# Kernel optimization log

Hardware: AMD Instinct MI355X
Metric: run time of the kernel (lower is better)

## Reference

```python
import jax, jax.numpy as jnp
import numpy as np

N_NODES = 200000
N_EDGES = 400000
N_GRAPHS = 4096
H = 300
L = 5
BN_EPS = 1e-5


def setup_inputs() -> dict:
    key = jax.random.key(0)
    ks = jax.random.split(key, 12)
    s = 0.05  # weight scale for numerical stability across 5 layers
    return {
        'x': jax.random.randint(ks[0], (N_NODES, 9), 0, 120),
        'edge_index': jax.random.randint(ks[1], (2, N_EDGES), 0, N_NODES),
        'edge_attr': jax.random.randint(ks[2], (N_EDGES, 3), 0, 16),
        'batch': jnp.sort(jax.random.randint(ks[3], (N_NODES,), 0, N_GRAPHS)),
        'atom_emb': jax.random.normal(ks[4], (9, 120, H), jnp.float32) * s,
        'bond_emb': jax.random.normal(ks[5], (L, 3, 16, H), jnp.float32) * s,
        'eps': jnp.zeros((L,), jnp.float32),
        'W1': jax.random.normal(ks[6], (L, H, 2 * H), jnp.float32) * s,
        'b1': jnp.zeros((L, 2 * H), jnp.float32),
        'bn_gamma': jnp.ones((L, 2 * H), jnp.float32),
        'bn_beta': jnp.zeros((L, 2 * H), jnp.float32),
        'bn_mean': jnp.zeros((L, 2 * H), jnp.float32),
        'bn_var': jnp.ones((L, 2 * H), jnp.float32),
        'W2': jax.random.normal(ks[7], (L, 2 * H, H), jnp.float32) * s,
        'b2': jnp.zeros((L, H), jnp.float32),
        'cls_W': jax.random.normal(ks[8], (H, 2), jnp.float32) * s,
        'cls_b': jnp.zeros((2,), jnp.float32),
    }


def reference(x, edge_index, edge_attr, batch, atom_emb, bond_emb, eps,
              W1, b1, bn_gamma, bn_beta, bn_mean, bn_var, W2, b2, cls_W, cls_b):
    N = x.shape[0]
    # AtomEncoder: sum of 9 categorical embeddings -> [N, H]
    h = jnp.sum(atom_emb[jnp.arange(9)[None, :], x], axis=1)
    src, dst = edge_index[0], edge_index[1]
    feat_idx3 = jnp.arange(3)[None, :]
    for l in range(W1.shape[0]):
        # BondEncoder for this layer: sum of 3 categorical embeddings -> [E, H]
        e = jnp.sum(bond_emb[l][feat_idx3, edge_attr], axis=1)
        # message = relu(x_j + edge_emb), aggregated by scatter-add at dst
        m = jax.nn.relu(h[src] + e)
        agg = jax.ops.segment_sum(m, dst, num_segments=N)
        z = (1.0 + eps[l]) * h + agg
        # MLP: Linear(H,2H) -> BN(eval) -> ReLU -> Linear(2H,H)
        z = z @ W1[l] + b1[l]
        z = (z - bn_mean[l]) * (bn_gamma[l] * jax.lax.rsqrt(bn_var[l] + BN_EPS)) + bn_beta[l]
        z = jax.nn.relu(z)
        h = z @ W2[l] + b2[l]
    # global mean pool over graphs
    sums = jax.ops.segment_sum(h, batch, num_segments=N_GRAPHS)
    counts = jax.ops.segment_sum(jnp.ones((N, 1), h.dtype), batch, num_segments=N_GRAPHS)
    graph_feature = sums / jnp.maximum(counts, 1.0)
    logits = graph_feature @ cls_W + cls_b
    return logits, graph_feature
```

## Files before the change

### kernel.cpp

```cpp
#include <hip/hip_runtime.h>
#include <hip/hip_bf16.h>

#define N_NODES 200000
#define N_EDGES 400000
#define N_GRAPHS 4096
#define HDIM 300
#define H2DIM 600
#define NLAYERS 5

typedef __hip_bfloat16 bf16;
typedef __attribute__((ext_vector_type(4))) short s16x4;
typedef __attribute__((ext_vector_type(8))) short s16x8;
typedef __attribute__((ext_vector_type(4))) float f32x4v;

__device__ inline short f2bf(float f) {
    __hip_bfloat16 b = __float2bfloat16(f);
    return *(short*)&b;
}
__device__ inline float bf2f(short s) {
    __hip_bfloat16 b = *(__hip_bfloat16*)&s;
    return __bfloat162float(b);
}

__global__ void diag_kernel(float* __restrict__ out, int n, float val) {
    int i = blockIdx.x * blockDim.x + threadIdx.x;
    if (i < n) out[i] = val;
}

__global__ void hist_kernel(const int* __restrict__ edge_index, int* __restrict__ offs) {
    int e = blockIdx.x * blockDim.x + threadIdx.x;
    if (e >= N_EDGES) return;
    atomicAdd(&offs[edge_index[N_EDGES + e]], 1);
}

#define SCAN_N 200001
__global__ void scan1_kernel(int* __restrict__ offs, int* __restrict__ bsum) {
    __shared__ int ls[256];
    int tid = threadIdx.x;
    int base = blockIdx.x * 1024 + tid * 4;
    int v[4];
#pragma unroll
    for (int j = 0; j < 4; j++) v[j] = (base + j < SCAN_N) ? offs[base + j] : 0;
    int t = v[0] + v[1] + v[2] + v[3];
    ls[tid] = t;
    __syncthreads();
    for (int off = 1; off < 256; off <<= 1) {
        int y = (tid >= off) ? ls[tid - off] : 0;
        __syncthreads();
        ls[tid] += y;
        __syncthreads();
    }
    int ex = ls[tid] - t;
#pragma unroll
    for (int j = 0; j < 4; j++) {
        if (base + j < SCAN_N) offs[base + j] = ex;
        ex += v[j];
    }
    if (tid == 255) bsum[blockIdx.x] = ls[255];
}

__global__ void scan2_kernel(int* __restrict__ bsum, int nb) {
    __shared__ int ls[256];
    int tid = threadIdx.x;
    int v = (tid < nb) ? bsum[tid] : 0;
    ls[tid] = v;
    __syncthreads();
    for (int off = 1; off < 256; off <<= 1) {
        int y = (tid >= off) ? ls[tid - off] : 0;
        __syncthreads();
        ls[tid] += y;
        __syncthreads();
    }
    if (tid < nb) bsum[tid] = ls[tid] - v;
}

__global__ void scan3_kernel(int* __restrict__ offs, const int* __restrict__ bsum) {
    int i = blockIdx.x * blockDim.x + threadIdx.x;
    if (i >= SCAN_N) return;
    offs[i] += bsum[i >> 10];
}

__global__ void scatter_kernel(const int* __restrict__ edge_index,
                               const int* __restrict__ edge_attr,
                               int* __restrict__ offs,
                               int* __restrict__ sidx) {
    int e = blockIdx.x * blockDim.x + threadIdx.x;
    if (e >= N_EDGES) return;
    int src = edge_index[e];
    int dst = edge_index[N_EDGES + e];
    int combo = edge_attr[e * 3 + 0] | (edge_attr[e * 3 + 1] << 4) | (edge_attr[e * 3 + 2] << 8);
    int pos = atomicAdd(&offs[dst], 1);
    sidx[pos] = src | (combo << 18);
}

__global__ void etab_kernel(const float* __restrict__ bond_l, short* __restrict__ etab) {
    int idx = blockIdx.x * blockDim.x + threadIdx.x;
    if (idx >= 4096 * 304) return;
    int combo = idx / 304;
    int c = idx - combo * 304;
    if (c >= HDIM) { etab[idx] = 0; return; }
    int a0 = combo & 15, a1 = (combo >> 4) & 15, a2 = combo >> 8;
    float v = bond_l[a0 * HDIM + c] + bond_l[16 * HDIM + a1 * HDIM + c]
            + bond_l[32 * HDIM + a2 * HDIM + c];
    etab[idx] = f2bf(v);
}

__global__ void prep_w_swz(const float* __restrict__ W1, const float* __restrict__ W2,
                           short* __restrict__ Wt1s, short* __restrict__ Wt2s) {
    int idx = blockIdx.x * blockDim.x + threadIdx.x;
    const int G1 = NLAYERS * 40 * 10 * 64;
    const int G2 = NLAYERS * 20 * 20 * 64;
    if (idx < G1) {
        int l = idx / (40 * 10 * 64);
        int r = idx - l * (40 * 10 * 64);
        int nt = r / (10 * 64);
        int r2 = r - nt * (10 * 64);
        int kb = r2 >> 6;
        int lane = r2 & 63;
        int n = nt * 16 + (lane & 15);
        int k0 = kb * 32 + (lane >> 4) * 8;
        s16x8 o;
#pragma unroll
        for (int j = 0; j < 8; j++) {
            int k = k0 + j;
            float v = (n < H2DIM && k < HDIM) ? W1[((size_t)l * HDIM + k) * H2DIM + n] : 0.f;
            o[j] = f2bf(v);
        }
        *(s16x8*)&Wt1s[(size_t)idx * 8] = o;
    } else if (idx < G1 + G2) {
        int t = idx - G1;
        int l = t / (20 * 20 * 64);
        int r = t - l * (20 * 20 * 64);
        int nt = r / (20 * 64);
        int r2 = r - nt * (20 * 64);
        int kb = r2 >> 6;
        int lane = r2 & 63;
        int n = nt * 16 + (lane & 15);
        int k0 = kb * 32 + (lane >> 4) * 8;
        s16x8 o;
#pragma unroll
        for (int j = 0; j < 8; j++) {
            int k = k0 + j;
            float v = (n < HDIM && k < H2DIM) ? W2[((size_t)l * H2DIM + k) * HDIM + n] : 0.f;
            o[j] = f2bf(v);
        }
        *(s16x8*)&Wt2s[(size_t)t * 8] = o;
    }
}

__global__ void atom_kernel(const int* __restrict__ x,
                            const float* __restrict__ atom_emb,
                            short* __restrict__ h) {
    int idx = blockIdx.x * blockDim.x + threadIdx.x;
    if (idx >= N_NODES * HDIM) return;
    int n = idx / HDIM;
    int c = idx - n * HDIM;
    const int* xr = x + n * 9;
    float s = 0.f;
#pragma unroll
    for (int f = 0; f < 9; f++) s += atom_emb[f * 120 * HDIM + xr[f] * HDIM + c];
    h[idx] = f2bf(s);
}

__launch_bounds__(256)
__global__ void agg_kernel(const short* __restrict__ h_in,
                           short* __restrict__ z,
                           const int* __restrict__ offs,
                           const int* __restrict__ sidx,
                           const short* __restrict__ etab,
                           const float* __restrict__ eps, int l) {
    int tid = threadIdx.x;
    int q = tid >> 4;
    int l16 = tid & 15;
    int n = blockIdx.x * 16 + q;
    float e1 = 1.f + eps[l];
    int beg = (n == 0) ? 0 : offs[n - 1];
    int end = offs[n];

    float4 acc[5];
#pragma unroll
    for (int j = 0; j < 5; j++) acc[j] = (float4){0.f, 0.f, 0.f, 0.f};
    bool tail = l16 < 11;
    int ctail = 256 + l16 * 4;

    int e = beg;
    for (; e + 2 <= end; e += 2) {
        int pk0 = sidx[e];
        int pk1 = sidx[e + 1];
        const short* hr0 = h_in + (size_t)(pk0 & 0x3FFFF) * HDIM;
        const short* er0 = etab + (((unsigned)pk0) >> 18) * 304;
        const short* hr1 = h_in + (size_t)(pk1 & 0x3FFFF) * HDIM;
        const short* er1 = etab + (((unsigned)pk1) >> 18) * 304;
        s16x4 hv0[5], ev0[5], hv1[5], ev1[5];
#pragma unroll
        for (int rep = 0; rep < 4; rep++) {
            int c = rep * 64 + l16 * 4;
            hv0[rep] = *(const s16x4*)(hr0 + c);
            ev0[rep] = *(const s16x4*)(er0 + c);
            hv1[rep] = *(const s16x4*)(hr1 + c);
            ev1[rep] = *(const s16x4*)(er1 + c);
        }
        if (tail) {
            hv0[4] = *(const s16x4*)(hr0 + ctail);
            ev0[4] = *(const s16x4*)(er0 + ctail);
            hv1[4] = *(const s16x4*)(hr1 + ctail);
            ev1[4] = *(const s16x4*)(er1 + ctail);
        }
#pragma unroll
        for (int rep = 0; rep < 5; rep++) {
            if (rep == 4 && !tail) continue;
            acc[rep].x += fmaxf(0.f, bf2f(hv0[rep].x) + bf2f(ev0[rep].x))
                        + fmaxf(0.f, bf2f(hv1[rep].x) + bf2f(ev1[rep].x));
            acc[rep].y += fmaxf(0.f, bf2f(hv0[rep].y) + bf2f(ev0[rep].y))
                        + fmaxf(0.f, bf2f(hv1[rep].y) + bf2f(ev1[rep].y));
            acc[rep].z += fmaxf(0.f, bf2f(hv0[rep].z) + bf2f(ev0[rep].z))
                        + fmaxf(0.f, bf2f(hv1[rep].z) + bf2f(ev1[rep].z));
            acc[rep].w += fmaxf(0.f, bf2f(hv0[rep].w) + bf2f(ev0[rep].w))
                        + fmaxf(0.f, bf2f(hv1[rep].w) + bf2f(ev1[rep].w));
        }
    }
    if (e < end) {
        int pk0 = sidx[e];
        const short* hr0 = h_in + (size_t)(pk0 & 0x3FFFF) * HDIM;
        const short* er0 = etab + (((unsigned)pk0) >> 18) * 304;
        s16x4 hv0[5], ev0[5];
#pragma unroll
        for (int rep = 0; rep < 4; rep++) {
            int c = rep * 64 + l16 * 4;
            hv0[rep] = *(const s16x4*)(hr0 + c);
            ev0[rep] = *(const s16x4*)(er0 + c);
        }
        if (tail) {
            hv0[4] = *(const s16x4*)(hr0 + ctail);
            ev0[4] = *(const s16x4*)(er0 + ctail);
        }
#pragma unroll
        for (int rep = 0; rep < 5; rep++) {
            if (rep == 4 && !tail) continue;
            acc[rep].x += fmaxf(0.f, bf2f(hv0[rep].x) + bf2f(ev0[rep].x));
            acc[rep].y += fmaxf(0.f, bf2f(hv0[rep].y) + bf2f(ev0[rep].y));
            acc[rep].z += fmaxf(0.f, bf2f(hv0[rep].z) + bf2f(ev0[rep].z));
            acc[rep].w += fmaxf(0.f, bf2f(hv0[rep].w) + bf2f(ev0[rep].w));
        }
    }

    const short* hn = h_in + (size_t)n * HDIM;
    short* zr = z + (size_t)n * HDIM;
#pragma unroll
    for (int rep = 0; rep < 5; rep++) {
        if (rep == 4 && !tail) continue;
        int c = rep < 4 ? rep * 64 + l16 * 4 : ctail;
        s16x4 hv = *(const s16x4*)(hn + c);
        s16x4 o;
        o.x = f2bf(fmaf(e1, bf2f(hv.x), acc[rep].x));
        o.y = f2bf(fmaf(e1, bf2f(hv.y), acc[rep].y));
        o.z = f2bf(fmaf(e1, bf2f(hv.z), acc[rep].z));
        o.w = f2bf(fmaf(e1, bf2f(hv.w), acc[rep].w));
        *(s16x4*)(zr + c) = o;
    }
}

#define ZST 328
#define WBUF_OFF (64 * ZST)
#define WBUF_SHORTS (20 * 64 * 8)
#define YS_OFF (WBUF_OFF + WBUF_SHORTS)
#define YST 136
#define LDS_SHORTS (YS_OFF + 64 * YST)

__launch_bounds__(256, 2)
__global__ void mlp_kernel(const short* __restrict__ zin,
                           short* __restrict__ hout,
                           const short* __restrict__ Wt1,
                           const short* __restrict__ Wt2,
                           const float* __restrict__ b1l,
                           const float* __restrict__ gammal,
                           const float* __restrict__ betal,
                           const float* __restrict__ meanl,
                           const float* __restrict__ varl,
                           const float* __restrict__ b2l) {
    __shared__ short lds[LDS_SHORTS];
    int tid = threadIdx.x;
    int wng = tid >> 6;
    int lane = tid & 63;
    int quad = lane >> 4;
    int l16 = lane & 15;
    int row0 = blockIdx.x * 64;

    for (int i = tid; i < 64 * 82; i += 256) {
        int r = i / 82;
        int ch = i - r * 82;
        int c = ch * 4;
        s16x4 v = {0, 0, 0, 0};
        if (c < HDIM) v = *(const s16x4*)&zin[(size_t)(row0 + r) * HDIM + c];
        *(s16x4*)&lds[r * ZST + c] = v;
    }

    f32x4v acc2[4][5];
#pragma unroll
    for (int rt = 0; rt < 4; rt++)
#pragma unroll
        for (int ct = 0; ct < 5; ct++) acc2[rt][ct] = (f32x4v){0.f, 0.f, 0.f, 0.f};

    for (int cc = 0; cc < 5; cc++) {
        f32x4v acc1[4][2];
#pragma unroll
        for (int rt = 0; rt < 4; rt++)
#pragma unroll
            for (int ct = 0; ct < 2; ct++) acc1[rt][ct] = (f32x4v){0.f, 0.f, 0.f, 0.f};

        for (int kbp = 0; kbp < 5; kbp++) {
            __syncthreads();
#pragma unroll
            for (int it = 0; it < 4; it++) {
                int i = tid + 256 * it;
                int nt = i >> 7;
                int r2 = i & 127;
                int kb2 = r2 >> 6;
                int ln = r2 & 63;
                s16x8 v = *(const s16x8*)&Wt1[(size_t)(((cc * 8 + nt) * 10 + kbp * 2 + kb2) * 64 + ln) * 8];
                *(s16x8*)&lds[WBUF_OFF + ((nt * 2 + kb2) * 64 + ln) * 8] = v;
            }
            __syncthreads();
#pragma unroll
            for (int kb2 = 0; kb2 < 2; kb2++) {
                int ks = (kbp * 2 + kb2) * 32 + quad * 8;
                s16x8 a[4];
#pragma unroll
                for (int rt = 0; rt < 4; rt++)
                    a[rt] = *(const s16x8*)&lds[(rt * 16 + l16) * ZST + ks];
#pragma unroll
                for (int ct = 0; ct < 2; ct++) {
                    int nt = wng * 2 + ct;
                    s16x8 b = *(const s16x8*)&lds[WBUF_OFF + ((nt * 2 + kb2) * 64 + lane) * 8];
#pragma unroll
                    for (int rt = 0; rt < 4; rt++)
                        acc1[rt][ct] = __builtin_amdgcn_mfma_f32_16x16x32_bf16(a[rt], b, acc1[rt][ct], 0, 0, 0);
                }
            }
        }
#pragma unroll
        for (int ct = 0; ct < 2; ct++) {
            int kc = wng * 32 + ct * 16 + l16;
            int col = cc * 128 + kc;
            bool valid = col < H2DIM;
            float s = 0.f, sh = 0.f;
            if (valid) {
                s = gammal[col] * rsqrtf(varl[col] + 1e-5f);
                sh = betal[col] + (b1l[col] - meanl[col]) * s;
            }
#pragma unroll
            for (int rt = 0; rt < 4; rt++)
#pragma unroll
                for (int rr = 0; rr < 4; rr++) {
                    float v = valid ? fmaxf(0.f, fmaf(acc1[rt][ct][rr], s, sh)) : 0.f;
                    lds[YS_OFF + (rt * 16 + quad * 4 + rr) * YST + kc] = f2bf(v);
                }
        }
#pragma unroll
        for (int kbl = 0; kbl < 4; kbl++) {
            __syncthreads();
#pragma unroll
            for (int it = 0; it < 5; it++) {
                int i = tid + 256 * it;
                int nt = i >> 6;
                int ln = i & 63;
                s16x8 v = *(const s16x8*)&Wt2[(size_t)((nt * 20 + cc * 4 + kbl) * 64 + ln) * 8];
                *(s16x8*)&lds[WBUF_OFF + (nt * 64 + ln) * 8] = v;
            }
            __syncthreads();
            int ks = kbl * 32 + quad * 8;
            s16x8 a[4];
#pragma unroll
            for (int rt = 0; rt < 4; rt++)
                a[rt] = *(const s16x8*)&lds[YS_OFF + (rt * 16 + l16) * YST + ks];
#pragma unroll
            for (int ct = 0; ct < 5; ct++) {
                int nt = wng * 5 + ct;
                s16x8 b = *(const s16x8*)&lds[WBUF_OFF + (nt * 64 + lane) * 8];
#pragma unroll
                for (int rt = 0; rt < 4; rt++)
                    acc2[rt][ct] = __builtin_amdgcn_mfma_f32_16x16x32_bf16(a[rt], b, acc2[rt][ct], 0, 0, 0);
            }
        }
    }
#pragma unroll
    for (int ct = 0; ct < 5; ct++) {
        int col = wng * 80 + ct * 16 + l16;
        if (col < HDIM) {
            float bb = b2l[col];
#pragma unroll
            for (int rt = 0; rt < 4; rt++)
#pragma unroll
                for (int rr = 0; rr < 4; rr++) {
                    int row = row0 + rt * 16 + quad * 4 + rr;
                    hout[(size_t)row * HDIM + col] = f2bf(acc2[rt][ct][rr] + bb);
                }
        }
    }
}

__device__ int lower_bound_dev(const int* a, int n, int v) {
    int lo = 0, hi = n;
    while (lo < hi) {
        int mid = (lo + hi) >> 1;
        if (a[mid] < v) lo = mid + 1; else hi = mid;
    }
    return lo;
}

__global__ void pool_kernel(const short* __restrict__ h,
                            const int* __restrict__ batch,
                            const float* __restrict__ cls_W,
                            const float* __restrict__ cls_b,
                            float* __restrict__ out) {
    __shared__ int seg[2];
    __shared__ float r0[256], r1[256];
    int g = blockIdx.x;
    int t = threadIdx.x;
    if (t == 0) {
        seg[0] = lower_bound_dev(batch, N_NODES, g);
        seg[1] = lower_bound_dev(batch, N_NODES, g + 1);
    }
    __syncthreads();
    int s = seg[0], e = seg[1];
    float cnt = (float)(e - s);
    float inv = 1.f / fmaxf(cnt, 1.f);
    float p0 = 0.f, p1 = 0.f;
    for (int c = t; c < HDIM; c += 256) {
        float sum = 0.f;
        for (int n = s; n < e; n++) sum += bf2f(h[(size_t)n * HDIM + c]);
        float gf = sum * inv;
        out[2 * N_GRAPHS + g * HDIM + c] = gf;
        p0 += gf * cls_W[c * 2 + 0];
        p1 += gf * cls_W[c * 2 + 1];
    }
    r0[t] = p0;
    r1[t] = p1;
    __syncthreads();
    for (int st = 128; st > 0; st >>= 1) {
        if (t < st) { r0[t] += r0[t + st]; r1[t] += r1[t + st]; }
        __syncthreads();
    }
    if (t == 0) {
        out[g * 2 + 0] = r0[0] + cls_b[0];
        out[g * 2 + 1] = r1[0] + cls_b[1];
    }
}

extern "C" void kernel_launch(void* const* d_in, const int* in_sizes, int n_in,
                              void* d_out, int out_size, void* d_ws, size_t ws_size,
                              hipStream_t stream) {
    const int* x          = (const int*)d_in[0];
    const int* edge_index = (const int*)d_in[1];
    const int* edge_attr  = (const int*)d_in[2];
    const int* batch      = (const int*)d_in[3];
    const float* atom_emb = (const float*)d_in[4];
    const float* bond_emb = (const float*)d_in[5];
    const float* eps      = (const float*)d_in[6];
    const float* W1       = (const float*)d_in[7];
    const float* b1       = (const float*)d_in[8];
    const float* bn_gamma = (const float*)d_in[9];
    const float* bn_beta  = (const float*)d_in[10];
    const float* bn_mean  = (const float*)d_in[11];
    const float* bn_var   = (const float*)d_in[12];
    const float* W2       = (const float*)d_in[13];
    const float* b2       = (const float*)d_in[14];
    const float* cls_W    = (const float*)d_in[15];
    const float* cls_b    = (const float*)d_in[16];
    float* out = (float*)d_out;

    char* base = (char*)d_ws;
    const size_t OFF_HA   = 0;
    const size_t OFF_HB   = 120000000;
    const size_t OFF_WT1  = 240000000;
    const size_t OFF_WT2  = 242048000;
    const size_t OFF_ETAB = 244096000;
    const size_t OFF_SIDX = 246586368;
    const size_t OFF_OFFS = 248186368;
    const size_t OFF_BSUM = 248986384;
    const size_t TOTAL    = 248987168;

    if (ws_size < TOTAL) {
        float mb = (float)(ws_size >> 20);
        diag_kernel<<<(out_size + 255) / 256, 256, 0, stream>>>(out, out_size, mb);
        return;
    }

    short* hA   = (short*)(base + OFF_HA);
    short* hB   = (short*)(base + OFF_HB);
    short* Wt1s = (short*)(base + OFF_WT1);
    short* Wt2s = (short*)(base + OFF_WT2);
    short* etab = (short*)(base + OFF_ETAB);
    int*   sidx = (int*)(base + OFF_SIDX);
    int*   offs = (int*)(base + OFF_OFFS);
    int*   bsum = (int*)(base + OFF_BSUM);

    hipMemsetAsync(offs, 0, SCAN_N * sizeof(int), stream);
    hist_kernel<<<(N_EDGES + 255) / 256, 256, 0, stream>>>(edge_index, offs);
    scan1_kernel<<<196, 256, 0, stream>>>(offs, bsum);
    scan2_kernel<<<1, 256, 0, stream>>>(bsum, 196);
    scan3_kernel<<<(SCAN_N + 255) / 256, 256, 0, stream>>>(offs, bsum);
    scatter_kernel<<<(N_EDGES + 255) / 256, 256, 0, stream>>>(edge_index, edge_attr, offs, sidx);

    {
        int total = NLAYERS * 40 * 10 * 64 + NLAYERS * 20 * 20 * 64;
        prep_w_swz<<<(total + 255) / 256, 256, 0, stream>>>(W1, W2, Wt1s, Wt2s);
    }
    atom_kernel<<<(N_NODES * HDIM + 255) / 256, 256, 0, stream>>>(x, atom_emb, hA);

    for (int l = 0; l < NLAYERS; l++) {
        etab_kernel<<<(4096 * 304 + 255) / 256, 256, 0, stream>>>(
            bond_emb + (size_t)l * 3 * 16 * HDIM, etab);
        agg_kernel<<<N_NODES / 16, 256, 0, stream>>>(
            hA, hB, offs, sidx, etab, eps, l);
        mlp_kernel<<<N_NODES / 64, 256, 0, stream>>>(
            hB, hA,
            Wt1s + (size_t)l * 640 * 320, Wt2s + (size_t)l * 320 * 640,
            b1 + l * H2DIM, bn_gamma + l * H2DIM, bn_beta + l * H2DIM,
            bn_mean + l * H2DIM, bn_var + l * H2DIM, b2 + l * HDIM);
    }

    pool_kernel<<<N_GRAPHS, 256, 0, stream>>>(hA, batch, cls_W, cls_b, out);
}
```

Baseline: 2.661 ms.

## Use direct global-to-LDS weight loads and vectorize atom, pool, and MLP stores

```diff
diff --git a/kernel.cpp b/kernel.cpp
--- a/kernel.cpp
+++ b/kernel.cpp
@@ -20,6 +20,13 @@
 __device__ inline float bf2f(short s) {
     __hip_bfloat16 b = *(__hip_bfloat16*)&s;
     return __bfloat162float(b);
+}
+
+__device__ inline void gload_lds16(const short* g, short* l) {
+    __builtin_amdgcn_global_load_lds(
+        (const __attribute__((address_space(1))) unsigned int*)g,
+        (__attribute__((address_space(3))) unsigned int*)l,
+        16, 0, 0);
 }
 
 __global__ void diag_kernel(float* __restrict__ out, int n, float val) {
@@ -151,15 +158,19 @@
 __global__ void atom_kernel(const int* __restrict__ x,
                             const float* __restrict__ atom_emb,
                             short* __restrict__ h) {
-    int idx = blockIdx.x * blockDim.x + threadIdx.x;
-    if (idx >= N_NODES * HDIM) return;
-    int n = idx / HDIM;
-    int c = idx - n * HDIM;
+    int i = blockIdx.x * blockDim.x + threadIdx.x;
+    if (i >= N_NODES * 75) return;
+    int n = i / 75;
+    int c = (i - n * 75) * 4;
     const int* xr = x + n * 9;
-    float s = 0.f;
-#pragma unroll
-    for (int f = 0; f < 9; f++) s += atom_emb[f * 120 * HDIM + xr[f] * HDIM + c];
-    h[idx] = f2bf(s);
+    float4 s = {0.f, 0.f, 0.f, 0.f};
+#pragma unroll
+    for (int f = 0; f < 9; f++) {
+        float4 v = *(const float4*)&atom_emb[(size_t)(f * 120 + xr[f]) * HDIM + c];
+        s.x += v.x; s.y += v.y; s.z += v.z; s.w += v.w;
+    }
+    s16x4 o = {f2bf(s.x), f2bf(s.y), f2bf(s.z), f2bf(s.w)};
+    *(s16x4*)&h[(size_t)n * HDIM + c] = o;
 }
 
 __launch_bounds__(256)
@@ -288,11 +299,9 @@
 
     for (int i = tid; i < 64 * 82; i += 256) {
         int r = i / 82;
-        int ch = i - r * 82;
-        int c = ch * 4;
-        s16x4 v = {0, 0, 0, 0};
-        if (c < HDIM) v = *(const s16x4*)&zin[(size_t)(row0 + r) * HDIM + c];
-        *(s16x4*)&lds[r * ZST + c] = v;
+        int p = (i - r * 82) * 4;
+        s16x4 v = *(const s16x4*)&zin[(size_t)(row0 + r) * HDIM + p];
+        *(s16x4*)&lds[r * ZST + p] = v;
     }
 
     f32x4v acc2[4][5];
@@ -311,14 +320,12 @@
         for (int kbp = 0; kbp < 5; kbp++) {
             __syncthreads();
 #pragma unroll
-            for (int it = 0; it < 4; it++) {
-                int i = tid + 256 * it;
-                int nt = i >> 7;
-                int r2 = i & 127;
-                int kb2 = r2 >> 6;
-                int ln = r2 & 63;
-                s16x8 v = *(const s16x8*)&Wt1[(size_t)(((cc * 8 + nt) * 10 + kbp * 2 + kb2) * 64 + ln) * 8];
-                *(s16x8*)&lds[WBUF_OFF + ((nt * 2 + kb2) * 64 + ln) * 8] = v;
+            for (int j = 0; j < 4; j++) {
+                int c = j * 4 + wng;
+                int nt_ = c >> 1, kb2 = c & 1;
+                const short* src = Wt1 +
+                    ((size_t)(((cc * 8 + nt_) * 10 + kbp * 2 + kb2) * 64) + lane) * 8;
+                gload_lds16(src, &lds[WBUF_OFF + c * 512]);
             }
             __syncthreads();
 #pragma unroll
@@ -330,8 +337,8 @@
                     a[rt] = *(const s16x8*)&lds[(rt * 16 + l16) * ZST + ks];
 #pragma unroll
                 for (int ct = 0; ct < 2; ct++) {
-                    int nt = wng * 2 + ct;
-                    s16x8 b = *(const s16x8*)&lds[WBUF_OFF + ((nt * 2 + kb2) * 64 + lane) * 8];
+                    int c = (wng * 2 + ct) * 2 + kb2;
+                    s16x8 b = *(const s16x8*)&lds[WBUF_OFF + c * 512 + lane * 8];
 #pragma unroll
                     for (int rt = 0; rt < 4; rt++)
                         acc1[rt][ct] = __builtin_amdgcn_mfma_f32_16x16x32_bf16(a[rt], b, acc1[rt][ct], 0, 0, 0);
@@ -360,12 +367,11 @@
         for (int kbl = 0; kbl < 4; kbl++) {
             __syncthreads();
 #pragma unroll
-            for (int it = 0; it < 5; it++) {
-                int i = tid + 256 * it;
-                int nt = i >> 6;
-                int ln = i & 63;
-                s16x8 v = *(const s16x8*)&Wt2[(size_t)((nt * 20 + cc * 4 + kbl) * 64 + ln) * 8];
-                *(s16x8*)&lds[WBUF_OFF + (nt * 64 + ln) * 8] = v;
+            for (int j = 0; j < 5; j++) {
+                int c = j * 4 + wng;
+                const short* src = Wt2 +
+                    ((size_t)((c * 20 + cc * 4 + kbl) * 64) + lane) * 8;
+                gload_lds16(src, &lds[WBUF_OFF + c * 512]);
             }
             __syncthreads();
             int ks = kbl * 32 + quad * 8;
@@ -375,8 +381,8 @@
                 a[rt] = *(const s16x8*)&lds[YS_OFF + (rt * 16 + l16) * YST + ks];
 #pragma unroll
             for (int ct = 0; ct < 5; ct++) {
-                int nt = wng * 5 + ct;
-                s16x8 b = *(const s16x8*)&lds[WBUF_OFF + (nt * 64 + lane) * 8];
+                int c = wng * 5 + ct;
+                s16x8 b = *(const s16x8*)&lds[WBUF_OFF + c * 512 + lane * 8];
 #pragma unroll
                 for (int rt = 0; rt < 4; rt++)
                     acc2[rt][ct] = __builtin_amdgcn_mfma_f32_16x16x32_bf16(a[rt], b, acc2[rt][ct], 0, 0, 0);
@@ -392,10 +398,14 @@
             for (int rt = 0; rt < 4; rt++)
 #pragma unroll
                 for (int rr = 0; rr < 4; rr++) {
-                    int row = row0 + rt * 16 + quad * 4 + rr;
-                    hout[(size_t)row * HDIM + col] = f2bf(acc2[rt][ct][rr] + bb);
+                    int r = rt * 16 + quad * 4 + rr;
+                    lds[r * HDIM + col] = f2bf(acc2[rt][ct][rr] + bb);
                 }
         }
+    }
+    __syncthreads();
+    for (int i = tid; i < 64 * 75; i += 256) {
+        *(s16x4*)&hout[(size_t)row0 * HDIM + i * 4] = *(const s16x4*)&lds[i * 4];
     }
 }
 
@@ -414,7 +424,7 @@
                             const float* __restrict__ cls_b,
                             float* __restrict__ out) {
     __shared__ int seg[2];
-    __shared__ float r0[256], r1[256];
+    __shared__ float r0s[256], r1s[256];
     int g = blockIdx.x;
     int t = threadIdx.x;
     if (t == 0) {
@@ -423,27 +433,35 @@
     }
     __syncthreads();
     int s = seg[0], e = seg[1];
-    float cnt = (float)(e - s);
-    float inv = 1.f / fmaxf(cnt, 1.f);
+    float inv = 1.f / fmaxf((float)(e - s), 1.f);
     float p0 = 0.f, p1 = 0.f;
-    for (int c = t; c < HDIM; c += 256) {
-        float sum = 0.f;
-        for (int n = s; n < e; n++) sum += bf2f(h[(size_t)n * HDIM + c]);
-        float gf = sum * inv;
-        out[2 * N_GRAPHS + g * HDIM + c] = gf;
-        p0 += gf * cls_W[c * 2 + 0];
-        p1 += gf * cls_W[c * 2 + 1];
-    }
-    r0[t] = p0;
-    r1[t] = p1;
+    if (t < 75) {
+        int c = t * 4;
+        float4 sum = {0.f, 0.f, 0.f, 0.f};
+        for (int n = s; n < e; n++) {
+            s16x4 v = *(const s16x4*)&h[(size_t)n * HDIM + c];
+            sum.x += bf2f(v.x);
+            sum.y += bf2f(v.y);
+            sum.z += bf2f(v.z);
+            sum.w += bf2f(v.w);
+        }
+        float4 gf = {sum.x * inv, sum.y * inv, sum.z * inv, sum.w * inv};
+        *(float4*)&out[2 * N_GRAPHS + (size_t)g * HDIM + c] = gf;
+        p0 = gf.x * cls_W[c * 2] + gf.y * cls_W[(c + 1) * 2]
+           + gf.z * cls_W[(c + 2) * 2] + gf.w * cls_W[(c + 3) * 2];
+        p1 = gf.x * cls_W[c * 2 + 1] + gf.y * cls_W[(c + 1) * 2 + 1]
+           + gf.z * cls_W[(c + 2) * 2 + 1] + gf.w * cls_W[(c + 3) * 2 + 1];
+    }
+    r0s[t] = p0;
+    r1s[t] = p1;
     __syncthreads();
     for (int st = 128; st > 0; st >>= 1) {
-        if (t < st) { r0[t] += r0[t + st]; r1[t] += r1[t + st]; }
+        if (t < st) { r0s[t] += r0s[t + st]; r1s[t] += r1s[t + st]; }
         __syncthreads();
     }
     if (t == 0) {
-        out[g * 2 + 0] = r0[0] + cls_b[0];
-        out[g * 2 + 1] = r1[0] + cls_b[1];
+        out[g * 2 + 0] = r0s[0] + cls_b[0];
+        out[g * 2 + 1] = r1s[0] + cls_b[1];
     }
 }
 
@@ -506,7 +524,7 @@
         int total = NLAYERS * 40 * 10 * 64 + NLAYERS * 20 * 20 * 64;
         prep_w_swz<<<(total + 255) / 256, 256, 0, stream>>>(W1, W2, Wt1s, Wt2s);
     }
-    atom_kernel<<<(N_NODES * HDIM + 255) / 256, 256, 0, stream>>>(x, atom_emb, hA);
+    atom_kernel<<<(N_NODES * 75 + 255) / 256, 256, 0, stream>>>(x, atom_emb, hA);
 
     for (int l = 0; l < NLAYERS; l++) {
         etab_kernel<<<(4096 * 304 + 255) / 256, 256, 0, stream>>>(
```

Result: faster. 2.406 ms (-9.6%).
